# Optimization experiments

Hardware: AMD Instinct MI355X
Metric: run time of the kernel (lower is better)

The kernel has to match this reference:

```python
import jax, jax.numpy as jnp
import numpy as np


def _lstm_scan(x_seq, W, b, batch, hidden):
    # x_seq: [T, B, D]; returns final (h, c)
    def step(carry, x_t):
        h, c = carry
        gates = jnp.concatenate([x_t, h], axis=1) @ W + b  # [B, 4H]
        f, i, o, g = jnp.split(gates, 4, axis=1)
        f = jax.nn.sigmoid(f)
        i = jax.nn.sigmoid(i)
        o = jax.nn.sigmoid(o)
        g = jnp.tanh(g)
        c_next = f * c + i * g
        h_next = o * jnp.tanh(c_next)
        return (h_next, c_next), None
    h0 = jnp.zeros((batch, hidden), dtype=x_seq.dtype)
    c0 = jnp.zeros((batch, hidden), dtype=x_seq.dtype)
    (h, c), _ = jax.lax.scan(step, (h0, c0), x_seq)
    return h


def setup_inputs() -> dict:
    key = jax.random.key(0)
    ks = jax.random.split(key, 6)
    B, T, D, H, O = 64, 1024, 256, 512, 128
    x = jax.random.normal(ks[0], (B, T, D), dtype=jnp.float32)
    W_f = jax.random.normal(ks[1], (D + H, 4 * H), dtype=jnp.float32) * 0.01
    b_f = jnp.zeros((4 * H,), dtype=jnp.float32)
    W_b = jax.random.normal(ks[2], (D + H, 4 * H), dtype=jnp.float32) * 0.01
    b_b = jnp.zeros((4 * H,), dtype=jnp.float32)
    # nn.Linear(2H, O): y = h @ W_fc + b_fc with W_fc stored as [2H, O]
    bound = 1.0 / np.sqrt(2 * H)
    W_fc = jax.random.uniform(ks[3], (2 * H, O), minval=-bound, maxval=bound, dtype=jnp.float32)
    b_fc = jax.random.uniform(ks[4], (O,), minval=-bound, maxval=bound, dtype=jnp.float32)
    return {"x": x, "W_f": W_f, "b_f": b_f, "W_b": W_b, "b_b": b_b, "W_fc": W_fc, "b_fc": b_fc}


def reference(x, W_f, b_f, W_b, b_b, W_fc, b_fc):
    B, T, D = x.shape
    H = W_f.shape[1] // 4
    x_t = jnp.transpose(x, (1, 0, 2))  # [T, B, D]
    h_fwd_last = _lstm_scan(x_t, W_f, b_f, B, H)           # forward: last h at t=T-1
    h_bwd_last = _lstm_scan(x_t[::-1], W_b, b_b, B, H)     # backward: last h (processed t=0 last)
    h = jnp.concatenate([h_fwd_last, h_bwd_last], axis=1)  # [B, 2H]
    return h @ W_fc + b_fc
```

## Files before the change

kernel.cpp:

```cpp
#include <hip/hip_runtime.h>
#include <hip/hip_bf16.h>
#include <stdint.h>

typedef __bf16  bf16x8 __attribute__((ext_vector_type(8)));
typedef float   f32x16 __attribute__((ext_vector_type(16)));

#define NB   64
#define NT   1024
#define ND   256
#define NH   512
#define NWGD 32

#define LDS_WFR   0
#define LDS_RED   98304
#define LDS_HOUT  (98304+17408)
#define LDS_BIAS  (98304+17408+2048)
#define LDS_TOTAL (98304+17408+2048+256)

static __device__ __forceinline__ unsigned long long agent_load_u64(const void* p) {
  return __hip_atomic_load((const unsigned long long*)p, __ATOMIC_RELAXED,
                           __HIP_MEMORY_SCOPE_AGENT);
}
static __device__ __forceinline__ void agent_store_u64(void* p, unsigned long long v) {
  __hip_atomic_store((unsigned long long*)p, v, __ATOMIC_RELAXED,
                     __HIP_MEMORY_SCOPE_AGENT);
}
static __device__ __forceinline__ float fast_sigmoid(float v) {
  return __builtin_amdgcn_rcpf(1.0f + __expf(-v));
}
static __device__ __forceinline__ float fast_tanh(float v) {
  return 1.0f - 2.0f * __builtin_amdgcn_rcpf(1.0f + __expf(2.0f * v));
}

__global__ __launch_bounds__(256, 1) void bilstm_persist(
    const float* __restrict__ x,
    const float* __restrict__ Wf, const float* __restrict__ bf_,
    const float* __restrict__ Wb, const float* __restrict__ bb_,
    __hip_bfloat16* __restrict__ hbuf, unsigned int* __restrict__ cnt)
{
  extern __shared__ char smem[];
  __bf16*         wfr   = (__bf16*)(smem + LDS_WFR);
  float*          red   = (float*) (smem + LDS_RED);
  __hip_bfloat16* hout  = (__hip_bfloat16*)(smem + LDS_HOUT);
  float*          biasl = (float*) (smem + LDS_BIAS);

  const int tid = threadIdx.x;
  const int bid = blockIdx.x;
  const int dir = bid >> 5;
  const int jsl = bid & 31;

  const float* W  = dir ? Wb  : Wf;
  const float* bi = dir ? bb_ : bf_;

  const int lane = tid & 63;
  const int wid  = tid >> 6;
  const int ni   = wid & 1;
  const int kh   = wid >> 1;
  const int hi   = lane >> 5;
  const int bcol = ni * 32 + (lane & 31);

  if (tid < 64) {
    biasl[tid] = bi[(tid & 3) * 512 + jsl * 16 + (tid >> 2)];
  }
  for (int i = tid; i < 48*2*64*8; i += 256) {
    const int ln = i & 63;
    const int r2 = i >> 6;
    const int v  = r2 & 7;
    const int m2 = (r2 >> 3) & 1;
    const int kk = r2 >> 4;
    const int k  = kk*16 + (ln >> 5)*8 + v;
    const int n  = m2*32 + (ln & 31);
    const int gcol = (n & 3)*512 + jsl*16 + (n >> 2);
    wfr[((size_t)(kk*2 + m2)*64 + ln)*8 + v] = (__bf16)W[(size_t)k*2048 + gcol];
  }
  __syncthreads();

  float biasr[2][16];
  #pragma unroll
  for (int mi = 0; mi < 2; ++mi)
    #pragma unroll
    for (int r = 0; r < 16; ++r)
      biasr[mi][r] = (kh == 0) ? biasl[mi*32 + (r & 3) + 8*(r >> 2) + 4*hi] : 0.0f;

  float creg[8];
  #pragma unroll
  for (int i = 0; i < 8; ++i) creg[i] = 0.0f;

  __hip_bfloat16* hb = hbuf + (size_t)dir * (2*NB*NH);
  unsigned int* mycnt = cnt + dir * NT;

  for (int t = 0; t < NT; ++t) {
    const int trow = dir ? (NT - 1 - t) : t;
    const __hip_bfloat16* hprev = hb + (size_t)(t & 1) * (NB*NH);
    __hip_bfloat16*       hnext = hb + (size_t)((t + 1) & 1) * (NB*NH);

    f32x16 acc0, acc1;
    #pragma unroll
    for (int r = 0; r < 16; ++r) { acc0[r] = biasr[0][r]; acc1[r] = biasr[1][r]; }

    const int kk0 = kh * 24;
    const float* xbase = x + ((size_t)bcol * NT + trow) * ND;
    const char*  hrow  = (const char*)(hprev + (size_t)bcol * NH);

    #pragma unroll 4
    for (int i = 0; i < 24; ++i) {
      const int kk = kk0 + i;
      const int k  = kk*16 + hi*8;
      bf16x8 bfr;
      if (k < ND) {
        const float4 xa = *(const float4*)(xbase + k);
        const float4 xb = *(const float4*)(xbase + k + 4);
        bfr[0]=(__bf16)xa.x; bfr[1]=(__bf16)xa.y; bfr[2]=(__bf16)xa.z; bfr[3]=(__bf16)xa.w;
        bfr[4]=(__bf16)xb.x; bfr[5]=(__bf16)xb.y; bfr[6]=(__bf16)xb.z; bfr[7]=(__bf16)xb.w;
      } else {
        union { unsigned long long q[2]; bf16x8 v; } u;
        const int off = (k - ND) * 2;
        u.q[0] = agent_load_u64(hrow + off);
        u.q[1] = agent_load_u64(hrow + off + 8);
        bfr = u.v;
      }
      const bf16x8 a0 = *(const bf16x8*)(wfr + ((size_t)(kk*2 + 0)*64 + lane)*8);
      const bf16x8 a1 = *(const bf16x8*)(wfr + ((size_t)(kk*2 + 1)*64 + lane)*8);
      acc0 = __builtin_amdgcn_mfma_f32_32x32x16_bf16(a0, bfr, acc0, 0, 0, 0);
      acc1 = __builtin_amdgcn_mfma_f32_32x32x16_bf16(a1, bfr, acc1, 0, 0, 0);
    }

    if (kh == 1) {
      #pragma unroll
      for (int r = 0; r < 16; ++r) {
        red[((ni*2 + 0)*64 + lane)*17 + r] = acc0[r];
        red[((ni*2 + 1)*64 + lane)*17 + r] = acc1[r];
      }
    }
    __syncthreads();
    if (kh == 0) {
      #pragma unroll
      for (int r = 0; r < 16; ++r) {
        acc0[r] += red[((ni*2 + 0)*64 + lane)*17 + r];
        acc1[r] += red[((ni*2 + 1)*64 + lane)*17 + r];
      }
      #pragma unroll
      for (int mi = 0; mi < 2; ++mi) {
        const f32x16 aa = mi ? acc1 : acc0;
        #pragma unroll
        for (int s = 0; s < 4; ++s) {
          const float fg = fast_sigmoid(aa[4*s+0]);
          const float ig = fast_sigmoid(aa[4*s+1]);
          const float og = fast_sigmoid(aa[4*s+2]);
          const float gg = fast_tanh   (aa[4*s+3]);
          const int   p  = mi*4 + s;
          const float cn = fg * creg[p] + ig * gg;
          creg[p] = cn;
          const float hv = og * fast_tanh(cn);
          hout[bcol*16 + (mi*8 + 2*s + hi)] = __float2bfloat16(hv);
        }
      }
    }
    __syncthreads();
    {
      const unsigned long long vv = ((const unsigned long long*)hout)[tid];
      const int b  = tid >> 2;
      const int u0 = (tid & 3) * 4;
      agent_store_u64(hnext + (size_t)b*NH + jsl*16 + u0, vv);
    }
    __syncthreads();
    if (tid == 0) {
      __hip_atomic_fetch_add(&mycnt[t], 1u, __ATOMIC_RELAXED, __HIP_MEMORY_SCOPE_AGENT);
      while (__hip_atomic_load(&mycnt[t], __ATOMIC_RELAXED, __HIP_MEMORY_SCOPE_AGENT) < NWGD) {
        __builtin_amdgcn_s_sleep(1);
      }
    }
    __syncthreads();
  }
}

__global__ __launch_bounds__(128) void fc_out(
    const __hip_bfloat16* __restrict__ hbuf, const float* __restrict__ Wfc,
    const float* __restrict__ bfc, float* __restrict__ out)
{
  __shared__ float hrow[2*NH];
  const int b = blockIdx.x, o = threadIdx.x;
  const __hip_bfloat16* hf  = hbuf + (size_t)b*NH;
  const __hip_bfloat16* hb2 = hbuf + (size_t)2*NB*NH + (size_t)b*NH;
  for (int i = o; i < NH; i += 128) {
    hrow[i]      = __bfloat162float(hf[i]);
    hrow[NH + i] = __bfloat162float(hb2[i]);
  }
  __syncthreads();
  float acc = bfc[o];
  for (int k = 0; k < 2*NH; ++k)
    acc = fmaf(hrow[k], Wfc[(size_t)k*128 + o], acc);
  out[b*128 + o] = acc;
}

extern "C" void kernel_launch(void* const* d_in, const int* in_sizes, int n_in,
                              void* d_out, int out_size, void* d_ws, size_t ws_size,
                              hipStream_t stream) {
  (void)in_sizes; (void)n_in; (void)out_size; (void)ws_size;
  const float* x   = (const float*)d_in[0];
  const float* Wf  = (const float*)d_in[1];
  const float* bf_ = (const float*)d_in[2];
  const float* Wb  = (const float*)d_in[3];
  const float* bb_ = (const float*)d_in[4];
  const float* Wfc = (const float*)d_in[5];
  const float* bfc = (const float*)d_in[6];
  float* out = (float*)d_out;

  __hip_bfloat16* hbuf = (__hip_bfloat16*)d_ws;
  unsigned int*   cnt  = (unsigned int*)((char*)d_ws + 2*2*NB*NH*2);

  hipMemsetAsync(d_ws, 0, 2*2*NB*NH*2 + 2*NT*4, stream);

  hipFuncSetAttribute((const void*)bilstm_persist,
                      hipFuncAttributeMaxDynamicSharedMemorySize, LDS_TOTAL);

  bilstm_persist<<<dim3(64), dim3(256), LDS_TOTAL, stream>>>(x, Wf, bf_, Wb, bb_, hbuf, cnt);
  fc_out<<<dim3(NB), dim3(128), 0, stream>>>(hbuf, Wfc, bfc, out);
}
```

Baseline: 10.25 ms.

## Overlap next-step input projection with barrier and use per-block flag polling

Moves the x-part of the gate matmul for step t+1 off the critical path so it runs after h is stored and before the next wait. The single counter plus spin barrier is replaced by per-workgroup monotonic flags, each polled by a wavefront lane, with release and acquire fences. The split-K reduction becomes symmetric so both K-halves of the waves share the gate nonlinearities. The goal is a shorter serial per-timestep latency, at the cost of more subtle memory-ordering correctness.

```diff
diff --git a/kernel.cpp b/kernel.cpp
--- a/kernel.cpp
+++ b/kernel.cpp
@@ -36,7 +36,7 @@
     const float* __restrict__ x,
     const float* __restrict__ Wf, const float* __restrict__ bf_,
     const float* __restrict__ Wb, const float* __restrict__ bb_,
-    __hip_bfloat16* __restrict__ hbuf, unsigned int* __restrict__ cnt)
+    __hip_bfloat16* __restrict__ hbuf, unsigned int* __restrict__ flags)
 {
   extern __shared__ char smem[];
   __bf16*         wfr   = (__bf16*)(smem + LDS_WFR);
@@ -75,80 +75,100 @@
   }
   __syncthreads();
 
-  float biasr[2][16];
+  float biasr[2][8];
   #pragma unroll
   for (int mi = 0; mi < 2; ++mi)
     #pragma unroll
-    for (int r = 0; r < 16; ++r)
-      biasr[mi][r] = (kh == 0) ? biasl[mi*32 + (r & 3) + 8*(r >> 2) + 4*hi] : 0.0f;
-
-  float creg[8];
+    for (int j = 0; j < 8; ++j) {
+      const int r = 8*kh + j;
+      biasr[mi][j] = biasl[mi*32 + (r & 3) + 8*(r >> 2) + 4*hi];
+    }
+
+  float creg[4];
   #pragma unroll
-  for (int i = 0; i < 8; ++i) creg[i] = 0.0f;
+  for (int i = 0; i < 4; ++i) creg[i] = 0.0f;
 
   __hip_bfloat16* hb = hbuf + (size_t)dir * (2*NB*NH);
-  unsigned int* mycnt = cnt + dir * NT;
-
-  for (int t = 0; t < NT; ++t) {
-    const int trow = dir ? (NT - 1 - t) : t;
-    const __hip_bfloat16* hprev = hb + (size_t)(t & 1) * (NB*NH);
-    __hip_bfloat16*       hnext = hb + (size_t)((t + 1) & 1) * (NB*NH);
-
-    f32x16 acc0, acc1;
+  unsigned int* myflag  = flags + (size_t)(dir*32 + jsl) * 16;
+  unsigned int* pollptr = flags + (size_t)(dir*32 + (lane & 31)) * 16;
+
+  f32x16 acc0, acc1;
+
+  {
     #pragma unroll
-    for (int r = 0; r < 16; ++r) { acc0[r] = biasr[0][r]; acc1[r] = biasr[1][r]; }
-
-    const int kk0 = kh * 24;
+    for (int r = 0; r < 16; ++r) { acc0[r] = 0.0f; acc1[r] = 0.0f; }
+    #pragma unroll
+    for (int j = 0; j < 8; ++j) { acc0[8*kh+j] = biasr[0][j]; acc1[8*kh+j] = biasr[1][j]; }
+    const int trow = dir ? (NT - 1) : 0;
     const float* xbase = x + ((size_t)bcol * NT + trow) * ND;
-    const char*  hrow  = (const char*)(hprev + (size_t)bcol * NH);
-
     #pragma unroll 4
-    for (int i = 0; i < 24; ++i) {
-      const int kk = kk0 + i;
+    for (int i = 0; i < 8; ++i) {
+      const int kk = kh*8 + i;
       const int k  = kk*16 + hi*8;
+      const float4 xa = *(const float4*)(xbase + k);
+      const float4 xb = *(const float4*)(xbase + k + 4);
       bf16x8 bfr;
-      if (k < ND) {
-        const float4 xa = *(const float4*)(xbase + k);
-        const float4 xb = *(const float4*)(xbase + k + 4);
-        bfr[0]=(__bf16)xa.x; bfr[1]=(__bf16)xa.y; bfr[2]=(__bf16)xa.z; bfr[3]=(__bf16)xa.w;
-        bfr[4]=(__bf16)xb.x; bfr[5]=(__bf16)xb.y; bfr[6]=(__bf16)xb.z; bfr[7]=(__bf16)xb.w;
-      } else {
-        union { unsigned long long q[2]; bf16x8 v; } u;
-        const int off = (k - ND) * 2;
-        u.q[0] = agent_load_u64(hrow + off);
-        u.q[1] = agent_load_u64(hrow + off + 8);
-        bfr = u.v;
-      }
+      bfr[0]=(__bf16)xa.x; bfr[1]=(__bf16)xa.y; bfr[2]=(__bf16)xa.z; bfr[3]=(__bf16)xa.w;
+      bfr[4]=(__bf16)xb.x; bfr[5]=(__bf16)xb.y; bfr[6]=(__bf16)xb.z; bfr[7]=(__bf16)xb.w;
       const bf16x8 a0 = *(const bf16x8*)(wfr + ((size_t)(kk*2 + 0)*64 + lane)*8);
       const bf16x8 a1 = *(const bf16x8*)(wfr + ((size_t)(kk*2 + 1)*64 + lane)*8);
       acc0 = __builtin_amdgcn_mfma_f32_32x32x16_bf16(a0, bfr, acc0, 0, 0, 0);
       acc1 = __builtin_amdgcn_mfma_f32_32x32x16_bf16(a1, bfr, acc1, 0, 0, 0);
     }
-
-    if (kh == 1) {
-      #pragma unroll
-      for (int r = 0; r < 16; ++r) {
-        red[((ni*2 + 0)*64 + lane)*17 + r] = acc0[r];
-        red[((ni*2 + 1)*64 + lane)*17 + r] = acc1[r];
+  }
+
+  #pragma unroll 1
+  for (int t = 0; t < NT; ++t) {
+    const __hip_bfloat16* hprev = hb + (size_t)(t & 1) * (NB*NH);
+    __hip_bfloat16*       hnext = hb + (size_t)((t + 1) & 1) * (NB*NH);
+
+    if (t) {
+      const unsigned int tgt = (unsigned int)t;
+      while (!__all((int)(__hip_atomic_load(pollptr, __ATOMIC_RELAXED,
+                                            __HIP_MEMORY_SCOPE_AGENT) >= tgt))) {}
+      __builtin_amdgcn_fence(__ATOMIC_ACQUIRE, "agent");
+    }
+
+    {
+      const char* hrow = (const char*)(hprev + (size_t)bcol * NH);
+      #pragma unroll 4
+      for (int i = 0; i < 16; ++i) {
+        const int kk = 16 + kh*16 + i;
+        const int off = (kk*16 + hi*8 - ND) * 2;
+        union { unsigned long long q[2]; bf16x8 v; } u;
+        u.q[0] = agent_load_u64(hrow + off);
+        u.q[1] = agent_load_u64(hrow + off + 8);
+        const bf16x8 a0 = *(const bf16x8*)(wfr + ((size_t)(kk*2 + 0)*64 + lane)*8);
+        const bf16x8 a1 = *(const bf16x8*)(wfr + ((size_t)(kk*2 + 1)*64 + lane)*8);
+        acc0 = __builtin_amdgcn_mfma_f32_32x32x16_bf16(a0, u.v, acc0, 0, 0, 0);
+        acc1 = __builtin_amdgcn_mfma_f32_32x32x16_bf16(a1, u.v, acc1, 0, 0, 0);
       }
     }
+
+    {
+      const int r0w = 8*(1-kh);
+      float* wslot = red + ((size_t)wid*64 + lane)*17;
+      #pragma unroll
+      for (int j = 0; j < 8; ++j) { wslot[j] = acc0[r0w+j]; wslot[8+j] = acc1[r0w+j]; }
+    }
     __syncthreads();
-    if (kh == 0) {
-      #pragma unroll
-      for (int r = 0; r < 16; ++r) {
-        acc0[r] += red[((ni*2 + 0)*64 + lane)*17 + r];
-        acc1[r] += red[((ni*2 + 1)*64 + lane)*17 + r];
-      }
+    {
+      const int r0 = 8*kh;
+      const float* rslot = red + ((size_t)(wid ^ 2)*64 + lane)*17;
+      #pragma unroll
+      for (int j = 0; j < 8; ++j) { acc0[r0+j] += rslot[j]; acc1[r0+j] += rslot[8+j]; }
+
       #pragma unroll
       for (int mi = 0; mi < 2; ++mi) {
         const f32x16 aa = mi ? acc1 : acc0;
         #pragma unroll
-        for (int s = 0; s < 4; ++s) {
+        for (int sl = 0; sl < 2; ++sl) {
+          const int s  = 2*kh + sl;
           const float fg = fast_sigmoid(aa[4*s+0]);
           const float ig = fast_sigmoid(aa[4*s+1]);
           const float og = fast_sigmoid(aa[4*s+2]);
           const float gg = fast_tanh   (aa[4*s+3]);
-          const int   p  = mi*4 + s;
+          const int   p  = mi*2 + sl;
           const float cn = fg * creg[p] + ig * gg;
           creg[p] = cn;
           const float hv = og * fast_tanh(cn);
@@ -157,20 +177,41 @@
       }
     }
     __syncthreads();
+
     {
       const unsigned long long vv = ((const unsigned long long*)hout)[tid];
-      const int b  = tid >> 2;
-      const int u0 = (tid & 3) * 4;
-      agent_store_u64(hnext + (size_t)b*NH + jsl*16 + u0, vv);
-    }
+      agent_store_u64(hnext + (size_t)(tid >> 2)*NH + jsl*16 + (tid & 3)*4, vv);
+    }
+
+    if (t + 1 < NT) {
+      #pragma unroll
+      for (int r = 0; r < 16; ++r) { acc0[r] = 0.0f; acc1[r] = 0.0f; }
+      #pragma unroll
+      for (int j = 0; j < 8; ++j) { acc0[8*kh+j] = biasr[0][j]; acc1[8*kh+j] = biasr[1][j]; }
+      const int trow = dir ? (NT - 2 - t) : (t + 1);
+      const float* xbase = x + ((size_t)bcol * NT + trow) * ND;
+      #pragma unroll 4
+      for (int i = 0; i < 8; ++i) {
+        const int kk = kh*8 + i;
+        const int k  = kk*16 + hi*8;
+        const float4 xa = *(const float4*)(xbase + k);
+        const float4 xb = *(const float4*)(xbase + k + 4);
+        bf16x8 bfr;
+        bfr[0]=(__bf16)xa.x; bfr[1]=(__bf16)xa.y; bfr[2]=(__bf16)xa.z; bfr[3]=(__bf16)xa.w;
+        bfr[4]=(__bf16)xb.x; bfr[5]=(__bf16)xb.y; bfr[6]=(__bf16)xb.z; bfr[7]=(__bf16)xb.w;
+        const bf16x8 a0 = *(const bf16x8*)(wfr + ((size_t)(kk*2 + 0)*64 + lane)*8);
+        const bf16x8 a1 = *(const bf16x8*)(wfr + ((size_t)(kk*2 + 1)*64 + lane)*8);
+        acc0 = __builtin_amdgcn_mfma_f32_32x32x16_bf16(a0, bfr, acc0, 0, 0, 0);
+        acc1 = __builtin_amdgcn_mfma_f32_32x32x16_bf16(a1, bfr, acc1, 0, 0, 0);
+      }
+    }
+
+    __builtin_amdgcn_fence(__ATOMIC_RELEASE, "agent");
     __syncthreads();
     if (tid == 0) {
-      __hip_atomic_fetch_add(&mycnt[t], 1u, __ATOMIC_RELAXED, __HIP_MEMORY_SCOPE_AGENT);
-      while (__hip_atomic_load(&mycnt[t], __ATOMIC_RELAXED, __HIP_MEMORY_SCOPE_AGENT) < NWGD) {
-        __builtin_amdgcn_s_sleep(1);
-      }
-    }
-    __syncthreads();
+      __hip_atomic_store(myflag, (unsigned int)(t + 1), __ATOMIC_RELAXED,
+                         __HIP_MEMORY_SCOPE_AGENT);
+    }
   }
 }
 
@@ -206,14 +247,14 @@
   const float* bfc = (const float*)d_in[6];
   float* out = (float*)d_out;
 
-  __hip_bfloat16* hbuf = (__hip_bfloat16*)d_ws;
-  unsigned int*   cnt  = (unsigned int*)((char*)d_ws + 2*2*NB*NH*2);
-
-  hipMemsetAsync(d_ws, 0, 2*2*NB*NH*2 + 2*NT*4, stream);
+  __hip_bfloat16* hbuf  = (__hip_bfloat16*)d_ws;
+  unsigned int*   flags = (unsigned int*)((char*)d_ws + 2*2*NB*NH*2);
+
+  hipMemsetAsync(d_ws, 0, 2*2*NB*NH*2 + 2*32*16*4, stream);
 
   hipFuncSetAttribute((const void*)bilstm_persist,
                       hipFuncAttributeMaxDynamicSharedMemorySize, LDS_TOTAL);
 
-  bilstm_persist<<<dim3(64), dim3(256), LDS_TOTAL, stream>>>(x, Wf, bf_, Wb, bb_, hbuf, cnt);
+  bilstm_persist<<<dim3(64), dim3(256), LDS_TOTAL, stream>>>(x, Wf, bf_, Wb, bb_, hbuf, flags);
   fc_out<<<dim3(NB), dim3(128), 0, stream>>>(hbuf, Wfc, bfc, out);
 }
```

Result: slower. 15.47 ms (+50.9%).
